# Kernel tuning notes

Hardware: AMD Instinct MI355X
Metric: run time of the kernel (lower is better)

The kernel has to match this reference:

```python
import jax, jax.numpy as jnp
import numpy as np

LOG2 = float(np.log(2.0))

def _ssp(x):
    # shifted softplus: ln(0.5*(exp(x)+1)) = softplus(x) - ln 2
    return jax.nn.softplus(x) - LOG2

def setup_inputs() -> dict:
    key = jax.random.key(0)
    ks = jax.random.split(key, 8)
    B, N, D = 32, 512, 1024
    H = D // 2
    s = lambda fan_in: 1.0 / np.sqrt(fan_in)
    return {
        "representation": jax.random.normal(ks[0], (B, N, D), jnp.float32),
        "R": jax.random.normal(ks[1], (B, N, 3), jnp.float32),
        "atom_mask": jnp.ones((B, N), jnp.float32),
        "W1": jax.random.normal(ks[2], (D, H), jnp.float32) * s(D),
        "b1": jnp.zeros((H,), jnp.float32),
        "W2": jax.random.normal(ks[3], (H, 1), jnp.float32) * s(H),
        "b2": jnp.zeros((1,), jnp.float32),
        "Wc1": jax.random.normal(ks[4], (D, H), jnp.float32) * s(D),
        "bc1": jnp.zeros((H,), jnp.float32),
        "Wc2": jax.random.normal(ks[5], (H, 1), jnp.float32) * s(H),
        "bc2": jnp.zeros((1,), jnp.float32),
    }

def reference(representation, R, atom_mask, W1, b1, W2, b2, Wc1, bc1, Wc2, bc2):
    B, N, _ = representation.shape
    # Atomwise pyramidal MLP: n_in -> n_in//2 (shifted softplus) -> 1
    yi = _ssp(jnp.einsum("bnd,dh->bnh", representation, W1) + b1)
    yi = jnp.einsum("bnh,ho->bno", yi, W2) + b2            # [B,N,1]
    # masked sum pool over atoms (mean=0, stddev=1 so standardize is identity)
    y = jnp.sum(yi * atom_mask[..., None], axis=1)          # [B,1]

    # pairwise distances with safe sqrt (diag is exactly zero)
    diff = R[:, None, :, :] - R[:, :, None, :]              # [B,N,N,3]
    d2 = jnp.sum(diff * diff, axis=-1)                      # [B,N,N]
    dist = jnp.where(d2 > 0, jnp.sqrt(jnp.where(d2 > 0, d2, 1.0)), 0.0)

    eye = jnp.eye(N, dtype=dist.dtype)
    tot_mask = atom_mask[:, None, :] * atom_mask[:, :, None] * (1.0 - eye)
    keep = (tot_mask != 0).astype(dist.dtype)               # [B,N,N]
    dist = dist * keep

    # charge net: Dense(n_in, n_in//2, ssp) -> Dense(n_in//2, 1)
    q = _ssp(jnp.einsum("bnd,dh->bnh", representation, Wc1) + bc1)
    q = jnp.einsum("bnh,ho->bno", q, Wc2) + bc2             # [B,N,1]

    inv2 = (1e-5 + dist) ** -2                              # [B,N,N]
    coulomb = q[:, :, 0][:, None, :] * inv2 * q             # [B,N,N] (q_j * inv * q_i)
    coulomb = coulomb * keep
    e = jnp.sum(coulomb, axis=(1, 2))                       # [B]

    return y + e[:, None]                                   # [B,1]
```

## Files before the change

kernel.cpp:

```cpp
#include <hip/hip_runtime.h>
#include <math.h>


typedef unsigned short u16;
typedef unsigned int u32;
typedef __bf16 bf16x8 __attribute__((ext_vector_type(8)));
typedef float f32x4 __attribute__((ext_vector_type(4)));

#define GK 1024
#define NT 16

#define GLOAD_LDS16(g, l) __builtin_amdgcn_global_load_lds( \
    (const __attribute__((address_space(1))) void*)(g),     \
    (__attribute__((address_space(3))) void*)(l), 16, 0, 0)

__device__ __forceinline__ u16 f2bf(float f) {
    u32 u = __float_as_uint(f);
    return (u16)((u + 0x7FFFu + ((u >> 16) & 1u)) >> 16);
}

__device__ __forceinline__ float ssp_f(float x) {
    return __logf(0.5f * (__expf(x) + 1.0f));
}

__device__ __forceinline__ float ssp_slow(float x) {
    return fmaxf(x, 0.0f) + log1pf(expf(-fabsf(x))) - 0.6931471805599453f;
}


__global__ __launch_bounds__(256) void prep(
    const float* __restrict__ rep, const float* __restrict__ W1,
    const float* __restrict__ Wc1, u16* __restrict__ Abf,
    u16* __restrict__ Btb, float* __restrict__ out)
{
    __shared__ float tile[32][33];
    const int blk = blockIdx.x;
    const int t = threadIdx.x;
    if (blk < 8192) {
        int i = (blk * 256 + t) * 8;
        float4 x = *(const float4*)(rep + i);
        float4 y = *(const float4*)(rep + i + 4);
        union { u16 h[8]; uint4 v; } o;
        o.h[0] = f2bf(x.x); o.h[1] = f2bf(x.y); o.h[2] = f2bf(x.z); o.h[3] = f2bf(x.w);
        o.h[4] = f2bf(y.x); o.h[5] = f2bf(y.y); o.h[6] = f2bf(y.z); o.h[7] = f2bf(y.w);
        *(uint4*)(Abf + i) = o.v;
        if (blk == 0 && t < 32) out[t] = 0.0f;
    } else {
        const int bb = blk - 8192;
        const int k0 = (bb & 31) * 32;
        const int n0 = (bb >> 5) * 32;
        const float* src = (n0 < 512) ? W1 : Wc1;
        const int ns0 = (n0 < 512) ? n0 : n0 - 512;
#pragma unroll
        for (int j = 0; j < 4; j++) {
            int idx = j * 256 + t;
            int kl = idx >> 5, nl = idx & 31;
            tile[kl][nl] = src[(size_t)(k0 + kl) * 512 + ns0 + nl];
        }
        __syncthreads();
#pragma unroll
        for (int j = 0; j < 4; j++) {
            int idx = j * 256 + t;
            int nl = idx >> 5, kl = idx & 31;
            Btb[(size_t)(n0 + nl) * 1024 + k0 + kl] = f2bf(tile[kl][nl]);
        }
    }
}


__global__ __launch_bounds__(512, 2) void gemm_mfma(
    const u16* __restrict__ A,
    const u16* __restrict__ Bt,
    const float* __restrict__ b1, const float* __restrict__ W2,
    const float* __restrict__ bc1, const float* __restrict__ Wc2,
    float* __restrict__ parts)
{
    __shared__ u16 smem[2][32768];

    const int blk = blockIdx.x;
    const int swz = ((blk & 7) << 5) | (blk >> 3);
    const int bm = swz >> 2;
    const int bn = swz & 3;
    const int tid = threadIdx.x;
    const int w = tid >> 6, lane = tid & 63;
    const int wm = w & 1, wn = w >> 1;
    const int lm = lane & 15, q = lane >> 4;

    f32x4 acc[8][4];
#pragma unroll
    for (int i = 0; i < 8; i++)
#pragma unroll
        for (int j = 0; j < 4; j++)
            acc[i][j] = (f32x4){0.0f, 0.0f, 0.0f, 0.0f};

    int goff[2][2];
#pragma unroll
    for (int h = 0; h < 2; h++)
#pragma unroll
        for (int p2 = 0; p2 < 2; p2++) {
            int ci = h * 1024 + (w * 2 + p2) * 64 + lane;
            int row = ci >> 3;
            int c = (ci & 7) ^ (row & 7);
            goff[h][p2] = row * GK + c * 8;
        }

    int arow[4], brow[2], aswz[2];
#pragma unroll
    for (int mi = 0; mi < 4; mi++) arow[mi] = (wm * 128 + mi * 16 + lm) * 64;
#pragma unroll
    for (int nj = 0; nj < 2; nj++) brow[nj] = (wn * 64 + nj * 16 + lm) * 64;
#pragma unroll
    for (int kk = 0; kk < 2; kk++) aswz[kk] = ((kk * 4 + q) ^ (lm & 7)) * 8;

    const u16* Ab = A + (size_t)bm * 256 * GK;
    const u16* Bb = Bt + (size_t)bn * 256 * GK;

#define STAGE_HT(G, RG, H, BUF) do {                                          \
    GLOAD_LDS16((G) + goff[H][0], &smem[BUF][(RG) + ((H) * 1024 + (w * 2 + 0) * 64) * 8]); \
    GLOAD_LDS16((G) + goff[H][1], &smem[BUF][(RG) + ((H) * 1024 + (w * 2 + 1) * 64) * 8]); \
} while (0)

#define READ_A(BUF, MH)                                                       \
    _Pragma("unroll") for (int mi = 0; mi < 4; mi++)                          \
    _Pragma("unroll") for (int kk = 0; kk < 2; kk++)                          \
        afr[mi][kk] = *(const bf16x8*)&smem[BUF][arow[mi] + (MH) * 4096 + aswz[kk]];

#define READ_B(BUF, NH, DST)                                                  \
    _Pragma("unroll") for (int nj = 0; nj < 2; nj++)                          \
    _Pragma("unroll") for (int kk = 0; kk < 2; kk++)                          \
        DST[nj][kk] = *(const bf16x8*)&smem[BUF][16384 + brow[nj] + (NH) * 2048 + aswz[kk]];

#define MFMA_QUAD(MH, NH, BF)                                                 \
    _Pragma("unroll") for (int kk = 0; kk < 2; kk++)                          \
    _Pragma("unroll") for (int mi = 0; mi < 4; mi++)                          \
    _Pragma("unroll") for (int nj = 0; nj < 2; nj++)                          \
        acc[(MH) * 4 + mi][(NH) * 2 + nj] = __builtin_amdgcn_mfma_f32_16x16x32_bf16( \
            afr[mi][kk], BF[nj][kk], acc[(MH) * 4 + mi][(NH) * 2 + nj], 0, 0, 0);

    STAGE_HT(Ab, 0, 0, 0);
    STAGE_HT(Bb, 16384, 0, 0);
    STAGE_HT(Bb, 16384, 1, 0);
    STAGE_HT(Ab, 0, 1, 0);
    asm volatile("s_waitcnt vmcnt(4)" ::: "memory");
    __builtin_amdgcn_s_barrier();

    bf16x8 afr[4][2], b0f[2][2], b1f[2][2];

    for (int t = 0; t < NT; ++t) {
        const int cur = t & 1, nxt = cur ^ 1;
        const u16* gA = Ab + ((t + 1) & (NT - 1)) * 64;
        const u16* gB = Bb + ((t + 1) & (NT - 1)) * 64;

        STAGE_HT(gA, 0, 0, nxt);
        READ_A(cur, 0);
        READ_B(cur, 0, b0f);
        __builtin_amdgcn_s_setprio(1);
        MFMA_QUAD(0, 0, b0f);
        __builtin_amdgcn_s_setprio(0);
        STAGE_HT(gB, 16384, 0, nxt);
        asm volatile("s_waitcnt vmcnt(6)" ::: "memory");
        __builtin_amdgcn_s_barrier();

        READ_B(cur, 1, b1f);
        __builtin_amdgcn_s_setprio(1);
        MFMA_QUAD(0, 1, b1f);
        __builtin_amdgcn_s_setprio(0);
        STAGE_HT(gB, 16384, 1, nxt);
        asm volatile("s_waitcnt vmcnt(6)" ::: "memory");
        __builtin_amdgcn_s_barrier();

        READ_A(cur, 1);
        __builtin_amdgcn_s_setprio(1);
        MFMA_QUAD(1, 1, b1f);
        __builtin_amdgcn_s_setprio(0);
        STAGE_HT(gA, 0, 1, nxt);
        __builtin_amdgcn_s_setprio(1);
        MFMA_QUAD(1, 0, b0f);
        __builtin_amdgcn_s_setprio(0);
        asm volatile("s_waitcnt vmcnt(4) lgkmcnt(0)" ::: "memory");
        __builtin_amdgcn_s_barrier();
    }
    asm volatile("s_waitcnt vmcnt(0)" ::: "memory");

#undef STAGE_HT
#undef READ_A
#undef READ_B
#undef MFMA_QUAD

    __syncthreads();
    float* red = (float*)&smem[0][0];
    const bool is_q = (bn >= 2);
    const float* bb2 = is_q ? bc1 : b1;
    const float* vv = is_q ? Wc2 : W2;
    float bias[4], v[4];
#pragma unroll
    for (int nfr = 0; nfr < 4; nfr++) {
        int c = (bn & 1) * 256 + wn * 64 + nfr * 16 + lm;
        bias[nfr] = bb2[c];
        v[nfr] = vv[c];
    }
#pragma unroll
    for (int mfr = 0; mfr < 8; mfr++) {
#pragma unroll
        for (int r = 0; r < 4; r++) {
            float s = 0.0f;
#pragma unroll
            for (int nfr = 0; nfr < 4; nfr++)
                s += v[nfr] * ssp_f(acc[mfr][nfr][r] + bias[nfr]);
            s += __shfl_xor(s, 1);
            s += __shfl_xor(s, 2);
            s += __shfl_xor(s, 4);
            s += __shfl_xor(s, 8);
            if (lm == 0) red[wn * 256 + wm * 128 + mfr * 16 + q * 4 + r] = s;
        }
    }
    __syncthreads();
    if (tid < 256) {
        float val = red[0 * 256 + tid] + red[1 * 256 + tid] +
                    red[2 * 256 + tid] + red[3 * 256 + tid];
        parts[(size_t)bn * 16384 + bm * 256 + tid] = val;
    }
}


__global__ __launch_bounds__(256) void coulomb_k(
    const float* __restrict__ R, const float* __restrict__ mask,
    const float* __restrict__ parts, const float* __restrict__ b2p,
    const float* __restrict__ bc2p, float* __restrict__ out)
{
    const int N = 512;
    const int b = blockIdx.y;
    const int chunk = blockIdx.x;
    __shared__ float Rx[512], Ry[512], Rz[512], QM[512];
    __shared__ float rbuf[4];
    const int tid = threadIdx.x;
    const float bc2 = bc2p[0];
    const float b2 = b2p[0];

    for (int j = tid; j < N; j += 256) {
        int idx = b * N + j;
        float m = mask[idx];
        const float* rp = R + (size_t)idx * 3;
        Rx[j] = rp[0];
        Ry[j] = rp[1];
        Rz[j] = rp[2];
        float qv = parts[2 * 16384 + idx] + parts[3 * 16384 + idx] + bc2;
        QM[j] = qv * m;
    }
    __syncthreads();

    const int i = chunk * 64 + (tid & 63);
    const int js = (tid >> 6) * 128;
    const float xi = Rx[i], yi = Ry[i], zi = Rz[i], qmi = QM[i];
    float e = 0.0f;
    for (int j = js; j < js + 128; j++) {
        float dx = xi - Rx[j];
        float dy = yi - Ry[j];
        float dz = zi - Rz[j];
        float d2 = dx * dx + dy * dy + dz * dz;
        float t = 1e-5f + sqrtf(d2);
        float term = qmi * QM[j] / (t * t);
        e += (j == i) ? 0.0f : term;
    }
    if (tid < 64) {
        int ii = b * N + chunk * 64 + tid;
        float yv = parts[0 * 16384 + ii] + parts[1 * 16384 + ii] + b2;
        e += yv * mask[ii];
    }
    for (int off = 32; off > 0; off >>= 1) e += __shfl_down(e, off, 64);
    if ((tid & 63) == 0) rbuf[tid >> 6] = e;
    __syncthreads();
    if (tid == 0) atomicAdd(&out[b], rbuf[0] + rbuf[1] + rbuf[2] + rbuf[3]);
}


#define BM 128
#define BN 64
#define BK 16

__global__ __launch_bounds__(256) void mlp_gemm(
    const float* __restrict__ A, const float* __restrict__ W1,
    const float* __restrict__ Wc1, const float* __restrict__ b1,
    const float* __restrict__ bc1, const float* __restrict__ W2,
    const float* __restrict__ Wc2, float* __restrict__ yi_part,
    float* __restrict__ q_part)
{
    const int K = 1024;
    const int bm = blockIdx.x;
    const int bn = blockIdx.y;
    const bool is_q = (bn >= 8);
    const float* __restrict__ W = is_q ? Wc1 : W1;
    const int j0 = (bn & 7) * BN;

    __shared__ float As[BK][BM + 4];
    __shared__ float Bs[BK][BN + 4];
    __shared__ float red[BM];

    const int tid = threadIdx.x;
    const int tx = tid & 15;
    const int ty = tid >> 4;

    float acc[8][4];
#pragma unroll
    for (int r = 0; r < 8; r++)
#pragma unroll
        for (int c = 0; c < 4; c++) acc[r][c] = 0.0f;

    const int a_row = tid >> 2;
    const int a_k4 = (tid & 3) * 4;
    const float* Arow0 = A + (size_t)(bm * BM + a_row) * K;
    const float* Arow1 = Arow0 + (size_t)64 * K;
    const int w_k = tid >> 4;
    const int w_j = (tid & 15) * 4;

    for (int kt = 0; kt < K; kt += BK) {
        float4 av0 = *(const float4*)(Arow0 + kt + a_k4);
        float4 av1 = *(const float4*)(Arow1 + kt + a_k4);
        float4 wv = *(const float4*)(W + (size_t)(kt + w_k) * 512 + j0 + w_j);
        __syncthreads();
        As[a_k4 + 0][a_row] = av0.x;
        As[a_k4 + 1][a_row] = av0.y;
        As[a_k4 + 2][a_row] = av0.z;
        As[a_k4 + 3][a_row] = av0.w;
        As[a_k4 + 0][a_row + 64] = av1.x;
        As[a_k4 + 1][a_row + 64] = av1.y;
        As[a_k4 + 2][a_row + 64] = av1.z;
        As[a_k4 + 3][a_row + 64] = av1.w;
        *(float4*)&Bs[w_k][w_j] = wv;
        __syncthreads();
#pragma unroll
        for (int kk = 0; kk < BK; kk++) {
            float4 a0 = *(const float4*)&As[kk][ty * 8];
            float4 a1 = *(const float4*)&As[kk][ty * 8 + 4];
            float4 bv = *(const float4*)&Bs[kk][tx * 4];
            float ar[8] = {a0.x, a0.y, a0.z, a0.w, a1.x, a1.y, a1.z, a1.w};
            float bc[4] = {bv.x, bv.y, bv.z, bv.w};
#pragma unroll
            for (int r = 0; r < 8; r++)
#pragma unroll
                for (int c = 0; c < 4; c++)
                    acc[r][c] = fmaf(ar[r], bc[c], acc[r][c]);
        }
    }

    const float* bb = is_q ? bc1 : b1;
    const float* vv = is_q ? Wc2 : W2;
    float bias[4], v[4];
#pragma unroll
    for (int c = 0; c < 4; c++) {
        bias[c] = bb[j0 + tx * 4 + c];
        v[c] = vv[j0 + tx * 4 + c];
    }
    if (tid < BM) red[tid] = 0.0f;
    __syncthreads();
#pragma unroll
    for (int r = 0; r < 8; r++) {
        float s = 0.0f;
#pragma unroll
        for (int c = 0; c < 4; c++)
            s += v[c] * ssp_slow(acc[r][c] + bias[c]);
        atomicAdd(&red[ty * 8 + r], s);
    }
    __syncthreads();
    float* target = is_q ? q_part : yi_part;
    if (tid < BM) atomicAdd(&target[(size_t)bm * BM + tid], red[tid]);
}

__global__ __launch_bounds__(256) void coulomb_fb(
    const float* __restrict__ R, const float* __restrict__ mask,
    const float* __restrict__ yi_part, const float* __restrict__ q_part,
    const float* __restrict__ b2p, const float* __restrict__ bc2p,
    float* __restrict__ out)
{
    const int N = 512;
    const int b = blockIdx.y;
    const int chunk = blockIdx.x;
    __shared__ float Rx[512], Ry[512], Rz[512], QM[512];
    __shared__ float rbuf[4];
    const int tid = threadIdx.x;
    const float bc2 = bc2p[0];
    const float b2 = b2p[0];

    for (int j = tid; j < N; j += 256) {
        float m = mask[b * N + j];
        const float* rp = R + ((size_t)b * N + j) * 3;
        Rx[j] = rp[0];
        Ry[j] = rp[1];
        Rz[j] = rp[2];
        QM[j] = (q_part[b * N + j] + bc2) * m;
    }
    __syncthreads();

    const int i = chunk * 64 + (tid & 63);
    const int js = (tid >> 6) * 128;
    const float xi = Rx[i], yi = Ry[i], zi = Rz[i], qmi = QM[i];
    float e = 0.0f;
    for (int j = js; j < js + 128; j++) {
        float dx = xi - Rx[j];
        float dy = yi - Ry[j];
        float dz = zi - Rz[j];
        float d2 = dx * dx + dy * dy + dz * dz;
        float t = 1e-5f + sqrtf(d2);
        float term = qmi * QM[j] / (t * t);
        e += (j == i) ? 0.0f : term;
    }
    if (tid < 64) {
        int ii = chunk * 64 + tid;
        e += (yi_part[b * N + ii] + b2) * mask[b * N + ii];
    }
    for (int off = 32; off > 0; off >>= 1) e += __shfl_down(e, off, 64);
    if ((tid & 63) == 0) rbuf[tid >> 6] = e;
    __syncthreads();
    if (tid == 0) atomicAdd(&out[b], rbuf[0] + rbuf[1] + rbuf[2] + rbuf[3]);
}


extern "C" void kernel_launch(void* const* d_in, const int* in_sizes, int n_in,
                              void* d_out, int out_size, void* d_ws, size_t ws_size,
                              hipStream_t stream) {
    const float* rep  = (const float*)d_in[0];
    const float* R    = (const float*)d_in[1];
    const float* mask = (const float*)d_in[2];
    const float* W1   = (const float*)d_in[3];
    const float* b1   = (const float*)d_in[4];
    const float* W2   = (const float*)d_in[5];
    const float* b2   = (const float*)d_in[6];
    const float* Wc1  = (const float*)d_in[7];
    const float* bc1  = (const float*)d_in[8];
    const float* Wc2  = (const float*)d_in[9];
    const float* bc2  = (const float*)d_in[10];
    float* out = (float*)d_out;

    const size_t szA = 16384ull * 1024 * 2;
    const size_t szB = 1024ull * 1024 * 2;
    const size_t szP = 8ull * 16384 * 4;
    const size_t need = szA + szB + szP;

    if (ws_size >= need) {
        u16* Abf = (u16*)d_ws;
        u16* Btb = (u16*)((char*)d_ws + szA);
        float* parts = (float*)((char*)d_ws + szA + szB);

        prep<<<8192 + 1024, 256, 0, stream>>>(rep, W1, Wc1, Abf, Btb, out);
        gemm_mfma<<<256, 512, 0, stream>>>(Abf, Btb, b1, W2, bc1, Wc2, parts);
        coulomb_k<<<dim3(8, 32), 256, 0, stream>>>(R, mask, parts, b2, bc2, out);
    } else {
        float* yi_part = (float*)d_ws;
        float* q_part = yi_part + 16384;
        hipMemsetAsync(d_ws, 0, 2 * 16384 * sizeof(float), stream);
        hipMemsetAsync(d_out, 0, 32 * sizeof(float), stream);
        mlp_gemm<<<dim3(128, 16), 256, 0, stream>>>(rep, W1, Wc1, b1, bc1, W2, Wc2,
                                                    yi_part, q_part);
        coulomb_fb<<<dim3(8, 32), 256, 0, stream>>>(R, mask, yi_part, q_part, b2, bc2, out);
    }
}
```

Measured before the change: 168.7 us.

## Load B fragments directly from global into registers, stage only A in LDS

The B operand (weights) is no longer staged through shared memory. Each wave loads its own B fragments straight from global memory into registers, double-buffered across k-tiles, while only A stays on the LDS async-copy path. This halves LDS usage and removes the B LDS reads and the intermediate barriers. The cost is uncoalesced-ish per-lane global loads of B, more registers for two B fragment buffers, and a full vmcnt(0) wait each tile, which reduces overlap.

```diff
diff --git a/kernel.cpp b/kernel.cpp
--- a/kernel.cpp
+++ b/kernel.cpp
@@ -75,7 +75,7 @@
     const float* __restrict__ bc1, const float* __restrict__ Wc2,
     float* __restrict__ parts)
 {
-    __shared__ u16 smem[2][32768];
+    __shared__ u16 smem[2][16384];
 
     const int blk = blockIdx.x;
     const int swz = ((blk & 7) << 5) | (blk >> 3);
@@ -104,88 +104,73 @@
             goff[h][p2] = row * GK + c * 8;
         }
 
-    int arow[4], brow[2], aswz[2];
+    int arow[4], aswz[2];
 #pragma unroll
     for (int mi = 0; mi < 4; mi++) arow[mi] = (wm * 128 + mi * 16 + lm) * 64;
 #pragma unroll
-    for (int nj = 0; nj < 2; nj++) brow[nj] = (wn * 64 + nj * 16 + lm) * 64;
-#pragma unroll
     for (int kk = 0; kk < 2; kk++) aswz[kk] = ((kk * 4 + q) ^ (lm & 7)) * 8;
 
     const u16* Ab = A + (size_t)bm * 256 * GK;
-    const u16* Bb = Bt + (size_t)bn * 256 * GK;
-
-#define STAGE_HT(G, RG, H, BUF) do {                                          \
-    GLOAD_LDS16((G) + goff[H][0], &smem[BUF][(RG) + ((H) * 1024 + (w * 2 + 0) * 64) * 8]); \
-    GLOAD_LDS16((G) + goff[H][1], &smem[BUF][(RG) + ((H) * 1024 + (w * 2 + 1) * 64) * 8]); \
+    const u16* Bw = Bt + (size_t)(bn * 256 + wn * 64 + lm) * GK + q * 8;
+
+#define STAGE_A(G, H, BUF) do {                                               \
+    GLOAD_LDS16((G) + goff[H][0], &smem[BUF][((H) * 1024 + (w * 2 + 0) * 64) * 8]); \
+    GLOAD_LDS16((G) + goff[H][1], &smem[BUF][((H) * 1024 + (w * 2 + 1) * 64) * 8]); \
 } while (0)
+
+#define LOAD_B(DST, KT)                                                       \
+    _Pragma("unroll") for (int nj = 0; nj < 4; nj++)                          \
+    _Pragma("unroll") for (int kk = 0; kk < 2; kk++)                          \
+        DST[nj][kk] = *(const bf16x8*)&Bw[(size_t)nj * 16 * GK + (KT) + kk * 32];
 
 #define READ_A(BUF, MH)                                                       \
     _Pragma("unroll") for (int mi = 0; mi < 4; mi++)                          \
     _Pragma("unroll") for (int kk = 0; kk < 2; kk++)                          \
         afr[mi][kk] = *(const bf16x8*)&smem[BUF][arow[mi] + (MH) * 4096 + aswz[kk]];
 
-#define READ_B(BUF, NH, DST)                                                  \
-    _Pragma("unroll") for (int nj = 0; nj < 2; nj++)                          \
-    _Pragma("unroll") for (int kk = 0; kk < 2; kk++)                          \
-        DST[nj][kk] = *(const bf16x8*)&smem[BUF][16384 + brow[nj] + (NH) * 2048 + aswz[kk]];
-
-#define MFMA_QUAD(MH, NH, BF)                                                 \
+#define MFMA_HALF(MH, BF)                                                     \
     _Pragma("unroll") for (int kk = 0; kk < 2; kk++)                          \
     _Pragma("unroll") for (int mi = 0; mi < 4; mi++)                          \
-    _Pragma("unroll") for (int nj = 0; nj < 2; nj++)                          \
-        acc[(MH) * 4 + mi][(NH) * 2 + nj] = __builtin_amdgcn_mfma_f32_16x16x32_bf16( \
-            afr[mi][kk], BF[nj][kk], acc[(MH) * 4 + mi][(NH) * 2 + nj], 0, 0, 0);
-
-    STAGE_HT(Ab, 0, 0, 0);
-    STAGE_HT(Bb, 16384, 0, 0);
-    STAGE_HT(Bb, 16384, 1, 0);
-    STAGE_HT(Ab, 0, 1, 0);
-    asm volatile("s_waitcnt vmcnt(4)" ::: "memory");
+    _Pragma("unroll") for (int nj = 0; nj < 4; nj++)                          \
+        acc[(MH) * 4 + mi][nj] = __builtin_amdgcn_mfma_f32_16x16x32_bf16(     \
+            afr[mi][kk], BF[nj][kk], acc[(MH) * 4 + mi][nj], 0, 0, 0);
+
+#define TILE_BODY(CUR, BCUR, BNXT, TNEXT_KT) do {                             \
+    const u16* gA_ = Ab + (TNEXT_KT);                                         \
+    STAGE_A(gA_, 0, (CUR) ^ 1);                                               \
+    STAGE_A(gA_, 1, (CUR) ^ 1);                                               \
+    LOAD_B(BNXT, (TNEXT_KT));                                                 \
+    READ_A(CUR, 0);                                                           \
+    __builtin_amdgcn_s_setprio(1);                                            \
+    MFMA_HALF(0, BCUR);                                                       \
+    __builtin_amdgcn_s_setprio(0);                                            \
+    READ_A(CUR, 1);                                                           \
+    __builtin_amdgcn_s_setprio(1);                                            \
+    MFMA_HALF(1, BCUR);                                                       \
+    __builtin_amdgcn_s_setprio(0);                                            \
+    asm volatile("s_waitcnt vmcnt(0) lgkmcnt(0)" ::: "memory");               \
+    __builtin_amdgcn_s_barrier();                                             \
+} while (0)
+
+    bf16x8 afr[4][2], bA[4][2], bB[4][2];
+
+    STAGE_A(Ab, 0, 0);
+    STAGE_A(Ab, 1, 0);
+    LOAD_B(bA, 0);
+    asm volatile("s_waitcnt vmcnt(0)" ::: "memory");
     __builtin_amdgcn_s_barrier();
 
-    bf16x8 afr[4][2], b0f[2][2], b1f[2][2];
-
-    for (int t = 0; t < NT; ++t) {
-        const int cur = t & 1, nxt = cur ^ 1;
-        const u16* gA = Ab + ((t + 1) & (NT - 1)) * 64;
-        const u16* gB = Bb + ((t + 1) & (NT - 1)) * 64;
-
-        STAGE_HT(gA, 0, 0, nxt);
-        READ_A(cur, 0);
-        READ_B(cur, 0, b0f);
-        __builtin_amdgcn_s_setprio(1);
-        MFMA_QUAD(0, 0, b0f);
-        __builtin_amdgcn_s_setprio(0);
-        STAGE_HT(gB, 16384, 0, nxt);
-        asm volatile("s_waitcnt vmcnt(6)" ::: "memory");
-        __builtin_amdgcn_s_barrier();
-
-        READ_B(cur, 1, b1f);
-        __builtin_amdgcn_s_setprio(1);
-        MFMA_QUAD(0, 1, b1f);
-        __builtin_amdgcn_s_setprio(0);
-        STAGE_HT(gB, 16384, 1, nxt);
-        asm volatile("s_waitcnt vmcnt(6)" ::: "memory");
-        __builtin_amdgcn_s_barrier();
-
-        READ_A(cur, 1);
-        __builtin_amdgcn_s_setprio(1);
-        MFMA_QUAD(1, 1, b1f);
-        __builtin_amdgcn_s_setprio(0);
-        STAGE_HT(gA, 0, 1, nxt);
-        __builtin_amdgcn_s_setprio(1);
-        MFMA_QUAD(1, 0, b0f);
-        __builtin_amdgcn_s_setprio(0);
-        asm volatile("s_waitcnt vmcnt(4) lgkmcnt(0)" ::: "memory");
-        __builtin_amdgcn_s_barrier();
-    }
-    asm volatile("s_waitcnt vmcnt(0)" ::: "memory");
-
-#undef STAGE_HT
+    for (int tt = 0; tt < NT / 2; ++tt) {
+        const int t0 = 2 * tt, t1 = 2 * tt + 1;
+        TILE_BODY(0, bA, bB, (((t0 + 1) & (NT - 1)) * 64));
+        TILE_BODY(1, bB, bA, (((t1 + 1) & (NT - 1)) * 64));
+    }
+
+#undef STAGE_A
+#undef LOAD_B
 #undef READ_A
-#undef READ_B
-#undef MFMA_QUAD
+#undef MFMA_HALF
+#undef TILE_BODY
 
     __syncthreads();
     float* red = (float*)&smem[0][0];
```

Result: slower. 188.5 us (+11.8%).
